# Optimization experiments

Measured on AMD Instinct MI355X. Metric: run time of the kernel, lower is better.

## Reference

```python
import jax, jax.numpy as jnp
import numpy as np

N_NODES = 100000
N_EDGES = 3200000
N_FEAT = 128
EMB = 64
HID = 64
N_SUB = 500000
N_GRAPHS = 1024
BN_EPS = 1e-5


def setup_inputs() -> dict:
    key = jax.random.key(0)
    ks = jax.random.split(key, 12)
    full_x = jax.random.normal(ks[0], (N_NODES, N_FEAT), dtype=jnp.float32)
    full_edge_index = jax.random.randint(ks[1], (2, N_EDGES), 0, N_NODES, dtype=jnp.int64)
    subgraph_node_indices = jax.random.randint(ks[2], (N_SUB,), 0, N_NODES, dtype=jnp.int64)
    batch_vector = jax.random.randint(ks[3], (N_SUB,), 0, N_GRAPHS, dtype=jnp.int64)
    # GCNConv params (glorot-style scale)
    W_enc = jax.random.normal(ks[4], (N_FEAT, EMB), dtype=jnp.float32) * (1.0 / np.sqrt(N_FEAT))
    b_enc = jnp.zeros((EMB,), dtype=jnp.float32)
    # predictor MLP params
    W1 = jax.random.normal(ks[5], (EMB, HID), dtype=jnp.float32) * (1.0 / np.sqrt(EMB))
    b1 = jnp.zeros((HID,), dtype=jnp.float32)
    gamma = jnp.ones((HID,), dtype=jnp.float32)
    beta = jnp.zeros((HID,), dtype=jnp.float32)
    W2 = jax.random.normal(ks[6], (HID, 1), dtype=jnp.float32) * (1.0 / np.sqrt(HID))
    b2 = jnp.zeros((1,), dtype=jnp.float32)
    return {
        "full_x": full_x,
        "full_edge_index": full_edge_index,
        "subgraph_node_indices": subgraph_node_indices,
        "batch_vector": batch_vector,
        "W_enc": W_enc, "b_enc": b_enc,
        "W1": W1, "b1": b1, "gamma": gamma, "beta": beta,
        "W2": W2, "b2": b2,
    }


def gcn_conv(x, edge_index, W, b):
    # PyG GCNConv: add self-loops, symmetric degree normalization, linear transform
    n = x.shape[0]
    loops = jnp.arange(n, dtype=edge_index.dtype)
    row = jnp.concatenate([edge_index[0], loops])  # source
    col = jnp.concatenate([edge_index[1], loops])  # target
    deg = jax.ops.segment_sum(jnp.ones_like(col, dtype=x.dtype), col, num_segments=n)
    dinv = jnp.where(deg > 0, jax.lax.rsqrt(deg), 0.0)
    norm = dinv[row] * dinv[col]  # [E+N]
    xw = x @ W  # transform first: [N, EMB]
    msgs = xw[row] * norm[:, None]
    out = jax.ops.segment_sum(msgs, col, num_segments=n)
    return out + b


def reference(full_x, full_edge_index, subgraph_node_indices, batch_vector,
              W_enc, b_enc, W1, b1, gamma, beta, W2, b2):
    # encoder + relu over all nodes
    h = jax.nn.relu(gcn_conv(full_x, full_edge_index, W_enc, b_enc))  # [N, EMB]
    # gather subgraph members
    sub = h[subgraph_node_indices]  # [N_SUB, EMB]
    # segment-mean pool into per-subgraph embeddings
    sums = jax.ops.segment_sum(sub, batch_vector, num_segments=N_GRAPHS)
    cnts = jax.ops.segment_sum(jnp.ones((sub.shape[0],), sub.dtype), batch_vector, num_segments=N_GRAPHS)
    pooled = sums / jnp.maximum(cnts, 1.0)[:, None]  # [N_GRAPHS, EMB]
    # predictor: Linear -> ReLU -> BatchNorm1d (training-mode batch stats) -> Linear
    z = jax.nn.relu(pooled @ W1 + b1)  # [N_GRAPHS, HID]
    mu = jnp.mean(z, axis=0)
    var = jnp.mean((z - mu) ** 2, axis=0)  # biased, as torch BN normalization
    zn = (z - mu) * jax.lax.rsqrt(var + BN_EPS) * gamma + beta
    return zn @ W2 + b2  # [N_GRAPHS, 1]
```

## Files before the change

### kernel.cpp

```cpp
#include <hip/hip_runtime.h>

#define N_NODES 100000
#define N_EDGES 3200000
#define N_FEAT 128
#define EMB 64
#define HID 64
#define N_SUB 500000
#define N_GRAPHS 1024
#define BN_EPS 1e-5f

#define NBKT 782
#define TILE 4096
#define NTILES 782
#define NGTILES 123
#define BKT_CAP 7168
#define GCAP 640
#define ZROW 100000
#define RPT 9

typedef __attribute__((ext_vector_type(8))) short short8;
typedef __attribute__((ext_vector_type(4))) float floatx4;

#define OFF_BCUR   0u
#define OFF_BCURG  4096u
#define OFF_BNSUM  8192u
#define ZERO_BYTES 8704u
#define OFF_DINV   12288u
#define OFF_OFFS   412672u
#define OFF_PAIRS  812672u
#define OFF_CSR    OFF_PAIRS
#define OFF_XWS    23235200u
#define OFF_SORTED 36035328u
#define OFF_H      38656768u
#define OFF_Z      51456896u

__device__ __forceinline__ bool is_bf(const unsigned* gamma_raw) {
  return (gamma_raw[0] & 0xFFFFu) != 0u;
}
__device__ __forceinline__ bool idx_is64(const int* subp) {
  return (subp[1] | subp[3] | subp[5] | subp[7]) == 0;
}
__device__ __forceinline__ float bf2f(ushort u) {
  union { unsigned i; float f; } v; v.i = ((unsigned)u) << 16; return v.f;
}
__device__ __forceinline__ ushort f2bf(float f) {
  union { float f; unsigned i; } v; v.f = f;
  unsigned lsb = (v.i >> 16) & 1u;
  v.i += 0x7FFFu + lsb;
  return (ushort)(v.i >> 16);
}
__device__ __forceinline__ float ld_f(const void* p, int i, bool bf) {
  return bf ? bf2f(((const ushort*)p)[i]) : ((const float*)p)[i];
}
__device__ __forceinline__ float lo_bf(unsigned d) {
  union { unsigned u; float f; } v; v.u = d << 16; return v.f;
}
__device__ __forceinline__ float hi_bf(unsigned d) {
  union { unsigned u; float f; } v; v.u = d & 0xFFFF0000u; return v.f;
}

__global__ __launch_bounds__(256) void k_scatsort(
    const int* e, const int* subp, const int* batch,
    int* bcur, unsigned* pairs, int* bcurg, int* sorted) {
  __shared__ int cnt[1024], lscan[1024], gbase[1024], wsum[4];
  __shared__ unsigned stage[TILE];
  __shared__ unsigned short stgb[TILE];
  bool w64 = idx_is64(subp);
  int tid = threadIdx.x, lane = tid & 63, wv = tid >> 6;
  bool edges = blockIdx.x < NTILES;
  int base = edges ? blockIdx.x * TILE : (blockIdx.x - NTILES) * TILE;
  int tot  = edges ? N_EDGES : N_SUB;
  int nb   = edges ? NBKT : N_GRAPHS;
  int tcnt = min(TILE, tot - base);
  int key[16], val[16];
  bool act = tid * 16 < tcnt;
  const int* kb = edges ? e : batch;
  const int* vb = edges ? e : subp;
  long long ko = edges ? (long long)N_EDGES : 0;
  if (act) {
    if (w64) {
      const int4* kp = (const int4*)kb + (ko + base) / 2 + tid * 8;
      const int4* vp = (const int4*)vb + base / 2 + tid * 8;
#pragma unroll
      for (int k = 0; k < 8; ++k) {
        int4 a = kp[k]; key[2 * k] = a.x; key[2 * k + 1] = a.z;
        int4 c = vp[k]; val[2 * k] = c.x; val[2 * k + 1] = c.z;
      }
    } else {
      const int4* kp = (const int4*)(kb + ko) + base / 4 + tid * 4;
      const int4* vp = (const int4*)vb + base / 4 + tid * 4;
#pragma unroll
      for (int k = 0; k < 4; ++k) {
        int4 a = kp[k];
        key[4 * k] = a.x; key[4 * k + 1] = a.y; key[4 * k + 2] = a.z; key[4 * k + 3] = a.w;
        int4 c = vp[k];
        val[4 * k] = c.x; val[4 * k + 1] = c.y; val[4 * k + 2] = c.z; val[4 * k + 3] = c.w;
      }
    }
  }
  for (int i = tid; i < 1024; i += 256) cnt[i] = 0;
  __syncthreads();
  if (act) {
#pragma unroll
    for (int k = 0; k < 16; ++k)
      atomicAdd(&cnt[edges ? (key[k] >> 7) : key[k]], 1);
  }
  __syncthreads();
  int b0 = tid * 4;
  int v0 = cnt[b0], v1 = cnt[b0 + 1], v2 = cnt[b0 + 2], v3 = cnt[b0 + 3];
  int s = v0 + v1 + v2 + v3, sc = s;
#pragma unroll
  for (int d = 1; d < 64; d <<= 1) {
    int t = __shfl_up(sc, d);
    if (lane >= d) sc += t;
  }
  if (lane == 63) wsum[wv] = sc;
  __syncthreads();
  int woff = 0;
#pragma unroll
  for (int w = 0; w < 4; ++w) woff += (w < wv) ? wsum[w] : 0;
  int excl = sc + woff - s;
  lscan[b0] = excl; lscan[b0 + 1] = excl + v0;
  lscan[b0 + 2] = excl + v0 + v1; lscan[b0 + 3] = excl + v0 + v1 + v2;
  __syncthreads();
  for (int b = tid; b < 1024; b += 256) {
    int c = (b < nb) ? cnt[b] : 0;
    gbase[b] = c ? (edges ? b * BKT_CAP + atomicAdd(&bcur[b], c)
                          : b * GCAP + atomicAdd(&bcurg[b], c)) : 0;
  }
  __syncthreads();
  for (int b = tid; b < 1024; b += 256) cnt[b] = 0;
  __syncthreads();
  if (act) {
#pragma unroll
    for (int k = 0; k < 16; ++k) {
      int b = edges ? (key[k] >> 7) : key[k];
      int r = atomicAdd(&cnt[b], 1);
      int p = lscan[b] + r;
      stage[p] = edges ? (((unsigned)(key[k] & 127) << 20) | (unsigned)val[k])
                       : (unsigned)val[k];
      stgb[p] = (unsigned short)b;
    }
  }
  __syncthreads();
  if (edges) {
    for (int j = tid; j < tcnt; j += 256) {
      int b = stgb[j];
      pairs[gbase[b] + (j - lscan[b])] = stage[j];
    }
  } else {
    for (int j = tid; j < tcnt; j += 256) {
      int b = stgb[j];
      sorted[gbase[b] + (j - lscan[b])] = (int)stage[j];
    }
  }
}

__global__ __launch_bounds__(512) void k_csr(
    const unsigned* __restrict__ pairs, const int* __restrict__ bcur,
    int* __restrict__ csr, unsigned* __restrict__ offs, float* __restrict__ dinv) {
  __shared__ int dl[128], loff[128], lcur[128];
  __shared__ int stage[BKT_CAP];
  __shared__ int ptot;
  int tid = threadIdx.x, b = blockIdx.x;
  if (tid < 128) dl[tid] = 0;
  __syncthreads();
  int s = b * BKT_CAP, cnt = bcur[b];
  unsigned pr[RPT];
#pragma unroll
  for (int k = 0; k < RPT; ++k) {
    int j = tid + k * 512;
    pr[k] = (j < cnt) ? pairs[s + j] : 0u;
  }
#pragma unroll
  for (int k = 0; k < RPT; ++k)
    if (tid + k * 512 < cnt) atomicAdd(&dl[pr[k] >> 20], 1);
  __syncthreads();
  int deg = 0, pd = 0;
  if (tid < 128) { deg = dl[tid]; pd = (deg + 31) & ~31; loff[tid] = pd; }
  __syncthreads();
  for (int d = 1; d < 128; d <<= 1) {
    int t = (tid >= d && tid < 128) ? loff[tid - d] : 0;
    __syncthreads();
    if (tid < 128) loff[tid] += t;
    __syncthreads();
  }
  if (tid < 128) {
    int excl = loff[tid] - pd;
    lcur[tid] = excl;
    int n = b * 128 + tid;
    if (n < N_NODES) {
      offs[n] = ((unsigned)(pd >> 5) << 24) | (unsigned)(s + excl);
      dinv[n] = rsqrtf((float)(deg + 1));
    }
    if (tid == 127) ptot = loff[127];
  }
  __syncthreads();
  int pt = ptot;
  for (int j = tid; j < pt; j += 512) stage[j] = ZROW;
  __syncthreads();
#pragma unroll
  for (int k = 0; k < RPT; ++k) {
    if (tid + k * 512 < cnt) {
      int pos = atomicAdd(&lcur[pr[k] >> 20], 1);
      stage[pos] = (int)(pr[k] & 0xFFFFF);
    }
  }
  __syncthreads();
  for (int j = tid; j < pt; j += 512) csr[s + j] = stage[j];
}

__global__ void k_gemm(const void* xraw, const void* Wraw, const unsigned* gamu,
                       const float* __restrict__ dinv, ushort* __restrict__ xws) {
  if (blockIdx.x == 0 && threadIdx.x < 32)
    ((unsigned*)xws)[(unsigned)ZROW * 32u + threadIdx.x] = 0u;
  bool bf = is_bf(gamu);
  const ushort* Wus = (const ushort*)Wraw;
  const float*  Wf  = (const float*)Wraw;
  int wv = threadIdx.x >> 6, lane = threadIdx.x & 63;
  int m = lane & 15, quad = lane >> 4;
  int c0 = wv * 16;
  short8 bfrag[4];
#pragma unroll
  for (int kc = 0; kc < 4; ++kc)
#pragma unroll
    for (int j = 0; j < 8; ++j) {
      int idx = (kc * 32 + quad * 8 + j) * EMB + c0 + m;
      bfrag[kc][j] = (short)(bf ? Wus[idx] : f2bf(Wf[idx]));
    }
  const ushort* xs = (const ushort*)xraw;
  const float*  xf = (const float*)xraw;
  for (int t = blockIdx.x; t < N_NODES / 16; t += gridDim.x) {
    int r0 = t * 16;
    floatx4 acc = {0.f, 0.f, 0.f, 0.f};
    if (bf) {
#pragma unroll
      for (int kc = 0; kc < 4; ++kc) {
        short8 a = *(const short8*)(xs + (r0 + m) * N_FEAT + kc * 32 + quad * 8);
        acc = __builtin_amdgcn_mfma_f32_16x16x32_bf16(a, bfrag[kc], acc, 0, 0, 0);
      }
    } else {
#pragma unroll
      for (int kc = 0; kc < 4; ++kc) {
        const float* ap = xf + (r0 + m) * N_FEAT + kc * 32 + quad * 8;
        float4 f0 = *(const float4*)ap, f1 = *(const float4*)(ap + 4);
        short8 a;
        a[0] = (short)f2bf(f0.x); a[1] = (short)f2bf(f0.y);
        a[2] = (short)f2bf(f0.z); a[3] = (short)f2bf(f0.w);
        a[4] = (short)f2bf(f1.x); a[5] = (short)f2bf(f1.y);
        a[6] = (short)f2bf(f1.z); a[7] = (short)f2bf(f1.w);
        acc = __builtin_amdgcn_mfma_f32_16x16x32_bf16(a, bfrag[kc], acc, 0, 0, 0);
      }
    }
#pragma unroll
    for (int r = 0; r < 4; ++r) {
      int row = r0 + quad * 4 + r;
      xws[row * EMB + c0 + m] = f2bf(acc[r] * dinv[row]);
    }
  }
}

#define ACCU(d) { aL0 += lo_bf(d.x); aH0 += hi_bf(d.x); aL1 += lo_bf(d.y); aH1 += hi_bf(d.y); \
                  aL2 += lo_bf(d.z); aH2 += hi_bf(d.z); aL3 += lo_bf(d.w); aH3 += hi_bf(d.w); }

__global__ void k_agg(const ushort* __restrict__ xws, const float* __restrict__ dinv,
                      const unsigned* __restrict__ offs, const int* __restrict__ csr,
                      const void* benc, const unsigned* gamu, ushort* __restrict__ h) {
  if (blockIdx.x == 0 && threadIdx.x < 32)
    ((unsigned*)h)[(unsigned)ZROW * 32u + threadIdx.x] = 0u;
  bool bf = is_bf(gamu);
  const uint4* xw4 = (const uint4*)xws;
  int wv = threadIdx.x >> 6, lane = threadIdx.x & 63;
  int e8 = lane >> 3, q = lane & 7;
  int n = blockIdx.x * 4 + wv;
  unsigned w = offs[n];
  int start = (int)(w & 0xFFFFFFu);
  int iters = (int)(w >> 24);
  float aL0 = 0.f, aH0 = 0.f, aL1 = 0.f, aH1 = 0.f, aL2 = 0.f, aH2 = 0.f, aL3 = 0.f, aH3 = 0.f;
  const int4* ip = (const int4*)(csr + start) + e8;
  for (int it = 0; it < iters; ++it) {
    int4 idx = ip[it * 8];
    uint4 u0 = xw4[idx.x * 8 + q];
    uint4 u1 = xw4[idx.y * 8 + q];
    uint4 u2 = xw4[idx.z * 8 + q];
    uint4 u3 = xw4[idx.w * 8 + q];
    ACCU(u0) ACCU(u1) ACCU(u2) ACCU(u3)
  }
#pragma unroll
  for (int msk = 8; msk < 64; msk <<= 1) {
    aL0 += __shfl_xor(aL0, msk); aH0 += __shfl_xor(aH0, msk);
    aL1 += __shfl_xor(aL1, msk); aH1 += __shfl_xor(aH1, msk);
    aL2 += __shfl_xor(aL2, msk); aH2 += __shfl_xor(aH2, msk);
    aL3 += __shfl_xor(aL3, msk); aH3 += __shfl_xor(aH3, msk);
  }
  if (e8 == 0) {
    float dn = dinv[n];
    uint4 us = xw4[n * 8 + q];
    ushort o[8];
    o[0] = f2bf(fmaxf((aL0 + lo_bf(us.x)) * dn + ld_f(benc, q * 8 + 0, bf), 0.f));
    o[1] = f2bf(fmaxf((aH0 + hi_bf(us.x)) * dn + ld_f(benc, q * 8 + 1, bf), 0.f));
    o[2] = f2bf(fmaxf((aL1 + lo_bf(us.y)) * dn + ld_f(benc, q * 8 + 2, bf), 0.f));
    o[3] = f2bf(fmaxf((aH1 + hi_bf(us.y)) * dn + ld_f(benc, q * 8 + 3, bf), 0.f));
    o[4] = f2bf(fmaxf((aL2 + lo_bf(us.z)) * dn + ld_f(benc, q * 8 + 4, bf), 0.f));
    o[5] = f2bf(fmaxf((aH2 + hi_bf(us.z)) * dn + ld_f(benc, q * 8 + 5, bf), 0.f));
    o[6] = f2bf(fmaxf((aL3 + lo_bf(us.w)) * dn + ld_f(benc, q * 8 + 6, bf), 0.f));
    o[7] = f2bf(fmaxf((aH3 + hi_bf(us.w)) * dn + ld_f(benc, q * 8 + 7, bf), 0.f));
    uint4 ov;
    ov.x = (unsigned)o[0] | ((unsigned)o[1] << 16);
    ov.y = (unsigned)o[2] | ((unsigned)o[3] << 16);
    ov.z = (unsigned)o[4] | ((unsigned)o[5] << 16);
    ov.w = (unsigned)o[6] | ((unsigned)o[7] << 16);
    ((uint4*)h)[n * 8 + q] = ov;
  }
}

__global__ void k_poolmlp1(const ushort* __restrict__ h, const int* __restrict__ sorted,
                           const int* __restrict__ bcurg, const void* W1, const void* b1,
                           const unsigned* gamu, float* __restrict__ z, float* bn) {
  bool bf = is_bf(gamu);
  __shared__ float red[4 * 64];
  __shared__ float pl[64];
  const uint4* h4 = (const uint4*)h;
  int g = blockIdx.x;
  int tid = threadIdx.x, wv = tid >> 6, lane = tid & 63;
  int e8 = lane >> 3, q = lane & 7;
  int start = g * GCAP, cnt = bcurg[g];
  int end = start + cnt;
  float aL0 = 0.f, aH0 = 0.f, aL1 = 0.f, aH1 = 0.f, aL2 = 0.f, aH2 = 0.f, aL3 = 0.f, aH3 = 0.f;
  for (int i = start + wv * 32; i < end; i += 128) {
#pragma unroll
    for (int c = 0; c < 4; ++c) {
      int idx = i + c * 8 + e8;
      int l = sorted[idx];
      int nn = (idx < end) ? l : ZROW;
      uint4 u = h4[nn * 8 + q];
      ACCU(u)
    }
  }
#pragma unroll
  for (int msk = 8; msk < 64; msk <<= 1) {
    aL0 += __shfl_xor(aL0, msk); aH0 += __shfl_xor(aH0, msk);
    aL1 += __shfl_xor(aL1, msk); aH1 += __shfl_xor(aH1, msk);
    aL2 += __shfl_xor(aL2, msk); aH2 += __shfl_xor(aH2, msk);
    aL3 += __shfl_xor(aL3, msk); aH3 += __shfl_xor(aH3, msk);
  }
  if (e8 == 0) {
    float* r = red + wv * 64 + q * 8;
    r[0] = aL0; r[1] = aH0; r[2] = aL1; r[3] = aH1;
    r[4] = aL2; r[5] = aH2; r[6] = aL3; r[7] = aH3;
  }
  __syncthreads();
  if (tid < 64) {
    float s = red[tid] + red[64 + tid] + red[128 + tid] + red[192 + tid];
    pl[tid] = s / fmaxf((float)cnt, 1.f);
  }
  __syncthreads();
  if (tid < 64) {
    int f = tid;
    float acc = ld_f(b1, f, bf);
#pragma unroll 8
    for (int k = 0; k < HID; ++k) acc += pl[k] * ld_f(W1, k * HID + f, bf);
    float zv = fmaxf(acc, 0.f);
    z[g * HID + f] = zv;
    atomicAdd(&bn[f], zv);
    atomicAdd(&bn[HID + f], zv * zv);
  }
}

__global__ void k_mlp2(const float* __restrict__ z, const float* __restrict__ bn,
                       const void* gmm, const void* beta, const void* W2, const void* b2,
                       const unsigned* gamu, void* out) {
  bool bf = is_bf(gamu);
  int wv = threadIdx.x >> 6, f = threadIdx.x & 63;
  int g = blockIdx.x * 4 + wv;
  float mu = bn[f] * (1.f / N_GRAPHS);
  float var = bn[HID + f] * (1.f / N_GRAPHS) - mu * mu;
  float zn = (z[g * HID + f] - mu) * rsqrtf(var + BN_EPS) * ld_f(gmm, f, bf) + ld_f(beta, f, bf);
  float val = zn * ld_f(W2, f, bf);
  for (int off = 32; off; off >>= 1) val += __shfl_down(val, off);
  if (f == 0) {
    val += ld_f(b2, 0, bf);
    if (bf) ((ushort*)out)[g] = f2bf(val);
    else    ((float*)out)[g]  = val;
  }
}

extern "C" void kernel_launch(void* const* d_in, const int* in_sizes, int n_in,
                              void* d_out, int out_size, void* d_ws, size_t ws_size,
                              hipStream_t stream) {
  const void* x_raw    = d_in[0];
  const int*  e_raw    = (const int*)d_in[1];
  const int*  sub_raw  = (const int*)d_in[2];
  const int*  bat_raw  = (const int*)d_in[3];
  const void* Wenc     = d_in[4];
  const void* benc     = d_in[5];
  const void* W1       = d_in[6];
  const void* b1       = d_in[7];
  const unsigned* gamu = (const unsigned*)d_in[8];
  const void* beta     = d_in[9];
  const void* W2       = d_in[10];
  const void* b2       = d_in[11];

  char* ws = (char*)d_ws;
  int*      bcur   = (int*)(ws + OFF_BCUR);
  int*      bcurg  = (int*)(ws + OFF_BCURG);
  float*    bnsum  = (float*)(ws + OFF_BNSUM);
  float*    dinv   = (float*)(ws + OFF_DINV);
  unsigned* offs   = (unsigned*)(ws + OFF_OFFS);
  unsigned* pairs  = (unsigned*)(ws + OFF_PAIRS);
  int*      csr    = (int*)(ws + OFF_CSR);
  ushort*   xws    = (ushort*)(ws + OFF_XWS);
  int*      sorted = (int*)(ws + OFF_SORTED);
  ushort*   h      = (ushort*)(ws + OFF_H);
  float*    z      = (float*)(ws + OFF_Z);

  hipMemsetAsync(ws, 0, ZERO_BYTES, stream);

  k_scatsort<<<NTILES + NGTILES, 256, 0, stream>>>(e_raw, sub_raw, bat_raw,
                                                   bcur, pairs, bcurg, sorted);
  k_csr     <<<NBKT, 512, 0, stream>>>(pairs, bcur, csr, offs, dinv);
  k_gemm    <<<1024, 256, 0, stream>>>(x_raw, Wenc, gamu, dinv, xws);
  k_agg     <<<N_NODES / 4, 256, 0, stream>>>(xws, dinv, offs, csr, benc, gamu, h);
  k_poolmlp1<<<N_GRAPHS, 256, 0, stream>>>(h, sorted, bcurg, W1, b1, gamu, z, bnsum);
  k_mlp2    <<<N_GRAPHS / 4, 256, 0, stream>>>(z, bnsum, gamu, beta, W2, b2, gamu, d_out);
}
```

Before: 280.6 us.

## Split node feature tables into four 16-column slices for cache-local gather aggregation

Stores xw and h as four column slices of 16 bf16 features each, so every slice table is a quarter of the size. The aggregation kernel is relaunched with 1024-thread blocks, and the blocks for a given slice are interleaved so that concurrent gathers touch a smaller working set that fits better in cache. CSR padding drops from 32 to 16 entries per node, which cuts wasted padded gathers. In exchange, each edge index is now read four times (once per slice), the gathers become narrower 8-byte loads, and the pooling kernel's h indexing is updated to match the new slice layout.

```diff
diff --git a/kernel.cpp b/kernel.cpp
--- a/kernel.cpp
+++ b/kernel.cpp
@@ -1,11 +1,11 @@
 #include <hip/hip_runtime.h>
 
 #define N_NODES 100000
-#define N_EDGES 3200000
 #define N_FEAT 128
 #define EMB 64
 #define HID 64
 #define N_SUB 500000
+#define N_EDGES 3200000
 #define N_GRAPHS 1024
 #define BN_EPS 1e-5f
 
@@ -13,10 +13,16 @@
 #define TILE 4096
 #define NTILES 782
 #define NGTILES 123
-#define BKT_CAP 7168
+#define BKT_CAP 5888
 #define GCAP 640
 #define ZROW 100000
 #define RPT 9
+#define NSLICE 4
+#define SROWS 100004
+#define SLICE_US (SROWS * 16)
+#define SLICE_U2 (SROWS * 4)
+#define SLICE_U4 (SROWS * 2)
+#define SLICE_DW (SROWS * 8)
 
 typedef __attribute__((ext_vector_type(8))) short short8;
 typedef __attribute__((ext_vector_type(4))) float floatx4;
@@ -29,10 +35,10 @@
 #define OFF_OFFS   412672u
 #define OFF_PAIRS  812672u
 #define OFF_CSR    OFF_PAIRS
-#define OFF_XWS    23235200u
-#define OFF_SORTED 36035328u
-#define OFF_H      38656768u
-#define OFF_Z      51456896u
+#define OFF_XWS    19228288u
+#define OFF_SORTED 32028800u
+#define OFF_H      34650240u
+#define OFF_Z      47450752u
 
 __device__ __forceinline__ bool is_bf(const unsigned* gamma_raw) {
   return (gamma_raw[0] & 0xFFFFu) != 0u;
@@ -177,7 +183,7 @@
     if (tid + k * 512 < cnt) atomicAdd(&dl[pr[k] >> 20], 1);
   __syncthreads();
   int deg = 0, pd = 0;
-  if (tid < 128) { deg = dl[tid]; pd = (deg + 31) & ~31; loff[tid] = pd; }
+  if (tid < 128) { deg = dl[tid]; pd = (deg + 15) & ~15; loff[tid] = pd; }
   __syncthreads();
   for (int d = 1; d < 128; d <<= 1) {
     int t = (tid >= d && tid < 128) ? loff[tid - d] : 0;
@@ -190,7 +196,7 @@
     lcur[tid] = excl;
     int n = b * 128 + tid;
     if (n < N_NODES) {
-      offs[n] = ((unsigned)(pd >> 5) << 24) | (unsigned)(s + excl);
+      offs[n] = ((unsigned)(pd >> 4) << 24) | (unsigned)(s + excl);
       dinv[n] = rsqrtf((float)(deg + 1));
     }
     if (tid == 127) ptot = loff[127];
@@ -212,8 +218,10 @@
 
 __global__ void k_gemm(const void* xraw, const void* Wraw, const unsigned* gamu,
                        const float* __restrict__ dinv, ushort* __restrict__ xws) {
-  if (blockIdx.x == 0 && threadIdx.x < 32)
-    ((unsigned*)xws)[(unsigned)ZROW * 32u + threadIdx.x] = 0u;
+  if (blockIdx.x == 0 && threadIdx.x < 32) {
+    int r = threadIdx.x >> 3, d = threadIdx.x & 7;
+    ((unsigned*)xws)[r * SLICE_DW + ZROW * 8 + d] = 0u;
+  }
   bool bf = is_bf(gamu);
   const ushort* Wus = (const ushort*)Wraw;
   const float*  Wf  = (const float*)Wraw;
@@ -230,6 +238,7 @@
     }
   const ushort* xs = (const ushort*)xraw;
   const float*  xf = (const float*)xraw;
+  ushort* xout = xws + wv * SLICE_US;
   for (int t = blockIdx.x; t < N_NODES / 16; t += gridDim.x) {
     int r0 = t * 16;
     floatx4 acc = {0.f, 0.f, 0.f, 0.f};
@@ -255,64 +264,59 @@
 #pragma unroll
     for (int r = 0; r < 4; ++r) {
       int row = r0 + quad * 4 + r;
-      xws[row * EMB + c0 + m] = f2bf(acc[r] * dinv[row]);
-    }
-  }
-}
-
-#define ACCU(d) { aL0 += lo_bf(d.x); aH0 += hi_bf(d.x); aL1 += lo_bf(d.y); aH1 += hi_bf(d.y); \
-                  aL2 += lo_bf(d.z); aH2 += hi_bf(d.z); aL3 += lo_bf(d.w); aH3 += hi_bf(d.w); }
-
-__global__ void k_agg(const ushort* __restrict__ xws, const float* __restrict__ dinv,
-                      const unsigned* __restrict__ offs, const int* __restrict__ csr,
-                      const void* benc, const unsigned* gamu, ushort* __restrict__ h) {
-  if (blockIdx.x == 0 && threadIdx.x < 32)
-    ((unsigned*)h)[(unsigned)ZROW * 32u + threadIdx.x] = 0u;
+      xout[row * 16 + m] = f2bf(acc[r] * dinv[row]);
+    }
+  }
+}
+
+__global__ __launch_bounds__(1024) void k_agg(
+    const ushort* __restrict__ xws, const float* __restrict__ dinv,
+    const unsigned* __restrict__ offs, const int* __restrict__ csr,
+    const void* benc, const unsigned* gamu, ushort* __restrict__ h) {
+  if (blockIdx.x == 0 && threadIdx.x < 32) {
+    int r = threadIdx.x >> 3, d = threadIdx.x & 7;
+    ((unsigned*)h)[r * SLICE_DW + ZROW * 8 + d] = 0u;
+  }
   bool bf = is_bf(gamu);
-  const uint4* xw4 = (const uint4*)xws;
-  int wv = threadIdx.x >> 6, lane = threadIdx.x & 63;
-  int e8 = lane >> 3, q = lane & 7;
-  int n = blockIdx.x * 4 + wv;
+  int tid = threadIdx.x, wv = tid >> 6, lane = tid & 63;
+  int m8 = blockIdx.x & 7;
+  int s = m8 >> 1, sub = m8 & 1;
+  int n = (((blockIdx.x >> 3) << 1) + sub) * 16 + wv;
+  int e = lane >> 2, q4 = lane & 3;
   unsigned w = offs[n];
   int start = (int)(w & 0xFFFFFFu);
   int iters = (int)(w >> 24);
-  float aL0 = 0.f, aH0 = 0.f, aL1 = 0.f, aH1 = 0.f, aL2 = 0.f, aH2 = 0.f, aL3 = 0.f, aH3 = 0.f;
-  const int4* ip = (const int4*)(csr + start) + e8;
+  const uint2* xb = (const uint2*)xws + (size_t)s * SLICE_U2;
+  const int* cp = csr + start + e;
+  float aL0 = 0.f, aH0 = 0.f, aL1 = 0.f, aH1 = 0.f;
   for (int it = 0; it < iters; ++it) {
-    int4 idx = ip[it * 8];
-    uint4 u0 = xw4[idx.x * 8 + q];
-    uint4 u1 = xw4[idx.y * 8 + q];
-    uint4 u2 = xw4[idx.z * 8 + q];
-    uint4 u3 = xw4[idx.w * 8 + q];
-    ACCU(u0) ACCU(u1) ACCU(u2) ACCU(u3)
-  }
-#pragma unroll
-  for (int msk = 8; msk < 64; msk <<= 1) {
+    int idx = cp[it * 16];
+    uint2 u = xb[idx * 4 + q4];
+    aL0 += lo_bf(u.x); aH0 += hi_bf(u.x);
+    aL1 += lo_bf(u.y); aH1 += hi_bf(u.y);
+  }
+#pragma unroll
+  for (int msk = 4; msk < 64; msk <<= 1) {
     aL0 += __shfl_xor(aL0, msk); aH0 += __shfl_xor(aH0, msk);
     aL1 += __shfl_xor(aL1, msk); aH1 += __shfl_xor(aH1, msk);
-    aL2 += __shfl_xor(aL2, msk); aH2 += __shfl_xor(aH2, msk);
-    aL3 += __shfl_xor(aL3, msk); aH3 += __shfl_xor(aH3, msk);
-  }
-  if (e8 == 0) {
+  }
+  if (lane < 4) {
     float dn = dinv[n];
-    uint4 us = xw4[n * 8 + q];
-    ushort o[8];
-    o[0] = f2bf(fmaxf((aL0 + lo_bf(us.x)) * dn + ld_f(benc, q * 8 + 0, bf), 0.f));
-    o[1] = f2bf(fmaxf((aH0 + hi_bf(us.x)) * dn + ld_f(benc, q * 8 + 1, bf), 0.f));
-    o[2] = f2bf(fmaxf((aL1 + lo_bf(us.y)) * dn + ld_f(benc, q * 8 + 2, bf), 0.f));
-    o[3] = f2bf(fmaxf((aH1 + hi_bf(us.y)) * dn + ld_f(benc, q * 8 + 3, bf), 0.f));
-    o[4] = f2bf(fmaxf((aL2 + lo_bf(us.z)) * dn + ld_f(benc, q * 8 + 4, bf), 0.f));
-    o[5] = f2bf(fmaxf((aH2 + hi_bf(us.z)) * dn + ld_f(benc, q * 8 + 5, bf), 0.f));
-    o[6] = f2bf(fmaxf((aL3 + lo_bf(us.w)) * dn + ld_f(benc, q * 8 + 6, bf), 0.f));
-    o[7] = f2bf(fmaxf((aH3 + hi_bf(us.w)) * dn + ld_f(benc, q * 8 + 7, bf), 0.f));
-    uint4 ov;
-    ov.x = (unsigned)o[0] | ((unsigned)o[1] << 16);
-    ov.y = (unsigned)o[2] | ((unsigned)o[3] << 16);
-    ov.z = (unsigned)o[4] | ((unsigned)o[5] << 16);
-    ov.w = (unsigned)o[6] | ((unsigned)o[7] << 16);
-    ((uint4*)h)[n * 8 + q] = ov;
-  }
-}
+    uint2 us = xb[n * 4 + lane];
+    int f0 = s * 16 + lane * 4;
+    ushort o0 = f2bf(fmaxf((aL0 + lo_bf(us.x)) * dn + ld_f(benc, f0 + 0, bf), 0.f));
+    ushort o1 = f2bf(fmaxf((aH0 + hi_bf(us.x)) * dn + ld_f(benc, f0 + 1, bf), 0.f));
+    ushort o2 = f2bf(fmaxf((aL1 + lo_bf(us.y)) * dn + ld_f(benc, f0 + 2, bf), 0.f));
+    ushort o3 = f2bf(fmaxf((aH1 + hi_bf(us.y)) * dn + ld_f(benc, f0 + 3, bf), 0.f));
+    uint2 ov;
+    ov.x = (unsigned)o0 | ((unsigned)o1 << 16);
+    ov.y = (unsigned)o2 | ((unsigned)o3 << 16);
+    ((uint2*)h)[(size_t)s * SLICE_U2 + n * 4 + lane] = ov;
+  }
+}
+
+#define ACCU(d) { aL0 += lo_bf(d.x); aH0 += hi_bf(d.x); aL1 += lo_bf(d.y); aH1 += hi_bf(d.y); \
+                  aL2 += lo_bf(d.z); aH2 += hi_bf(d.z); aL3 += lo_bf(d.w); aH3 += hi_bf(d.w); }
 
 __global__ void k_poolmlp1(const ushort* __restrict__ h, const int* __restrict__ sorted,
                            const int* __restrict__ bcurg, const void* W1, const void* b1,
@@ -324,6 +328,7 @@
   int g = blockIdx.x;
   int tid = threadIdx.x, wv = tid >> 6, lane = tid & 63;
   int e8 = lane >> 3, q = lane & 7;
+  size_t hb = (size_t)(q >> 1) * SLICE_U4 + (q & 1);
   int start = g * GCAP, cnt = bcurg[g];
   int end = start + cnt;
   float aL0 = 0.f, aH0 = 0.f, aL1 = 0.f, aH1 = 0.f, aL2 = 0.f, aH2 = 0.f, aL3 = 0.f, aH3 = 0.f;
@@ -333,7 +338,7 @@
       int idx = i + c * 8 + e8;
       int l = sorted[idx];
       int nn = (idx < end) ? l : ZROW;
-      uint4 u = h4[nn * 8 + q];
+      uint4 u = h4[hb + nn * 2];
       ACCU(u)
     }
   }
@@ -420,7 +425,7 @@
                                                    bcur, pairs, bcurg, sorted);
   k_csr     <<<NBKT, 512, 0, stream>>>(pairs, bcur, csr, offs, dinv);
   k_gemm    <<<1024, 256, 0, stream>>>(x_raw, Wenc, gamu, dinv, xws);
-  k_agg     <<<N_NODES / 4, 256, 0, stream>>>(xws, dinv, offs, csr, benc, gamu, h);
+  k_agg     <<<25000, 1024, 0, stream>>>(xws, dinv, offs, csr, benc, gamu, h);
   k_poolmlp1<<<N_GRAPHS, 256, 0, stream>>>(h, sorted, bcurg, W1, b1, gamu, z, bnsum);
   k_mlp2    <<<N_GRAPHS / 4, 256, 0, stream>>>(z, bnsum, gamu, beta, W2, b2, gamu, d_out);
 }
```

New measurement: 388.7 us. +38.5%, slower.
